# Performance work log

Measured on AMD Instinct MI355X. Metric: run time of the kernel, lower is better.

The kernel has to match this reference:

```python
import jax, jax.numpy as jnp
import numpy as np

B, S, HID = 2, 2048, 2048
H, HKV, D = 16, 4, 128
BS = 64            # block_size
TAU = 0.5          # threshold_tau
NB = S // BS       # number of blocks
SCALE = 1.0 / (D ** 0.5)


def _rotate_half(x):
    x1, x2 = x[..., : D // 2], x[..., D // 2 :]
    return jnp.concatenate([-x2, x1], axis=-1)


def setup_inputs() -> dict:
    key = jax.random.key(0)
    k0, k1, k2, k3, k4 = jax.random.split(key, 5)
    hidden_states = jax.random.normal(k0, (B, S, HID), jnp.float32)
    # standard rotary embeddings, [B, S, D] (ndim==3 path of _apply_rotary_pos_emb)
    pos = jnp.arange(S, dtype=jnp.float32)
    inv_freq = 1.0 / (10000.0 ** (jnp.arange(0, D, 2, dtype=jnp.float32) / D))
    emb = jnp.concatenate([pos[:, None] * inv_freq[None, :]] * 2, axis=-1)  # [S, D]
    cos = jnp.broadcast_to(jnp.cos(emb)[None], (B, S, D)).astype(jnp.float32)
    sin = jnp.broadcast_to(jnp.sin(emb)[None], (B, S, D)).astype(jnp.float32)
    Wq = jax.random.normal(k1, (HID, H * D), jnp.float32) * 0.02
    Wk = jax.random.normal(k2, (HID, HKV * D), jnp.float32) * 0.02
    Wv = jax.random.normal(k3, (HID, HKV * D), jnp.float32) * 0.02
    Wo = jax.random.normal(k4, (HID, HID), jnp.float32) * 0.02
    return {"hidden_states": hidden_states, "cos": cos, "sin": sin,
            "Wq": Wq, "Wk": Wk, "Wv": Wv, "Wo": Wo}


def reference(hidden_states, cos, sin, Wq, Wk, Wv, Wo):
    # QKV projections -> [B, heads, S, D]
    q = (hidden_states @ Wq).reshape(B, S, H, D).transpose(0, 2, 1, 3)
    k = (hidden_states @ Wk).reshape(B, S, HKV, D).transpose(0, 2, 1, 3)
    v = (hidden_states @ Wv).reshape(B, S, HKV, D).transpose(0, 2, 1, 3)
    # RoPE (cos/sin [B,S,D] -> broadcast over heads)
    c, s = cos[:, None], sin[:, None]
    q = q * c + _rotate_half(q) * s
    k = k * c + _rotate_half(k) * s
    # GQA repeat_interleave on head dim
    n_rep = H // HKV
    k = jnp.repeat(k, n_rep, axis=1)
    v = jnp.repeat(v, n_rep, axis=1)
    # ---- AttnGate: block-mean pooled Q/K scores -> hard block mask ----
    q_blk = q.reshape(B, H, NB, BS, D).mean(axis=3)  # [B,H,NB,D]
    k_blk = k.reshape(B, H, NB, BS, D).mean(axis=3)
    gate_logits = jnp.einsum('bhid,bhjd->bhij', q_blk, k_blk) * SCALE
    hard = jax.nn.sigmoid(gate_logits) >= TAU                      # [B,H,NB,NB]
    hard = hard | jnp.eye(NB, dtype=bool)                          # keep diagonal blocks
    hard = hard & jnp.tril(jnp.ones((NB, NB), dtype=bool))         # block-causal
    # expand block mask to token level and intersect with causal mask
    tok_mask = jnp.repeat(jnp.repeat(hard, BS, axis=2), BS, axis=3)  # [B,H,S,S]
    tok_mask = tok_mask & jnp.tril(jnp.ones((S, S), dtype=bool))
    # ---- block-sparse (masked) attention ----
    scores = jnp.einsum('bhsd,bhtd->bhst', q, k) * SCALE
    scores = jnp.where(tok_mask, scores, jnp.float32(-1e30))
    probs = jax.nn.softmax(scores.astype(jnp.float32), axis=-1).astype(v.dtype)
    out = jnp.einsum('bhst,bhtd->bhsd', probs, v)
    out = out.transpose(0, 2, 1, 3).reshape(B, S, HID)
    return out @ Wo
```

## Files before the change

### kernel.cpp

```cpp
#include <hip/hip_runtime.h>
#include <stdint.h>

typedef unsigned short u16;
typedef _Float16 half8 __attribute__((ext_vector_type(8)));
typedef float floatx4 __attribute__((ext_vector_type(4)));
typedef u16 u16x4 __attribute__((ext_vector_type(4)));

#define B_ 2
#define S_ 2048
#define HID_ 2048
#define H_ 16
#define HKV_ 4
#define D_ 128
#define NB_ 32
#define SCALE_ 0.08838834764831845f
#define SC_L2 0.12753102331884178f
#define SMAX_L2 5.770780163555852f

__device__ __forceinline__ u16 f2h_bits(float f) {
  _Float16 h = (_Float16)f;
  return __builtin_bit_cast(u16, h);
}

__global__ __launch_bounds__(256) void k_split_hs(const float* __restrict__ hs, u16* __restrict__ A2) {
  int idx = blockIdx.x * 256 + threadIdx.x;
  int f0 = idx * 4;
  float4 v = *reinterpret_cast<const float4*>(hs + f0);
  float vv[4] = {v.x, v.y, v.z, v.w};
  u16x4 h0, h1;
#pragma unroll
  for (int e = 0; e < 4; ++e) {
    _Float16 a = (_Float16)vv[e];
    float r = vv[e] - (float)a;
    _Float16 b = (_Float16)r;
    h0[e] = __builtin_bit_cast(u16, a);
    h1[e] = __builtin_bit_cast(u16, b);
  }
  int row = f0 >> 11;
  int col = f0 & 2047;
  *reinterpret_cast<u16x4*>(A2 + (size_t)row * 4096 + col) = h0;
  *reinterpret_cast<u16x4*>(A2 + (size_t)row * 4096 + 2048 + col) = h1;
}

__global__ __launch_bounds__(256) void k_transpose_split(const float* __restrict__ src, u16* __restrict__ dst,
                                                         int Kdim, int N, int ldd, int nsplit) {
  __shared__ float tile[64][65];
  int k0 = blockIdx.x * 64, n0 = blockIdx.y * 64;
#pragma unroll
  for (int p = 0; p < 16; ++p) {
    int e = threadIdx.x + p * 256;
    int r = e >> 6, c = e & 63;
    tile[r][c] = src[(size_t)(k0 + r) * N + n0 + c];
  }
  __syncthreads();
#pragma unroll
  for (int p = 0; p < 16; ++p) {
    int e = threadIdx.x + p * 256;
    int k = e & 63, n = e >> 6;
    float v = tile[k][n];
    for (int s = 0; s < nsplit; ++s) {
      _Float16 hh = (_Float16)v;
      dst[(size_t)(n0 + n) * ldd + s * Kdim + k0 + k] = __builtin_bit_cast(u16, hh);
      v -= (float)hh;
    }
  }
}


#define FENCE() __builtin_amdgcn_sched_barrier(0)
#define BAR() do { FENCE(); __builtin_amdgcn_s_barrier(); FENCE(); } while (0)
#define WAITVM(N) do { FENCE(); asm volatile("s_waitcnt vmcnt(" #N ")" ::: "memory"); FENCE(); } while (0)

__device__ __forceinline__ int kmap(int map, int t) {
  return ((map >> ((t >> 5) * 4)) & 15) * 2048 + (t & 31) * 64;
}

__device__ __forceinline__ void stage_half(const u16* __restrict__ src, int sr0, int lda, int kb,
                                           u16* dst, int w, int lane) {
#pragma unroll
  for (int rr = 0; rr < 2; ++rr) {
    int chunk = rr * 8 + w;
    int row = chunk * 8 + (lane >> 3);
    int slot = (lane & 7) ^ (lane >> 3);
    const u16* gp = src + (size_t)(sr0 + row) * lda + kb + slot * 8;
    __builtin_amdgcn_global_load_lds((const __attribute__((address_space(1))) unsigned int*)gp,
                                     (__attribute__((address_space(3))) unsigned int*)(dst + chunk * 512),
                                     16, 0, 0);
  }
}

#define RD_A(mh) do { \
  _Pragma("unroll") \
  for (int m_ = 0; m_ < 4; ++m_) { \
    aF[m_][0] = *reinterpret_cast<const half8*>(&sm[(mh)*8192 + (wm*64 + m_*16 + l15)*64 + ((quad ^ l7) * 8)]); \
    aF[m_][1] = *reinterpret_cast<const half8*>(&sm[(mh)*8192 + (wm*64 + m_*16 + l15)*64 + (((4 + quad) ^ l7) * 8)]); \
  } } while (0)

#define RD_B(nh, BF) do { \
  _Pragma("unroll") \
  for (int n_ = 0; n_ < 2; ++n_) { \
    BF[n_][0] = *reinterpret_cast<const half8*>(&sm[16384 + (nh)*8192 + (wn*32 + n_*16 + l15)*64 + ((quad ^ l7) * 8)]); \
    BF[n_][1] = *reinterpret_cast<const half8*>(&sm[16384 + (nh)*8192 + (wn*32 + n_*16 + l15)*64 + (((4 + quad) ^ l7) * 8)]); \
  } } while (0)

#define MM(mh, nh, BF) do { \
  __builtin_amdgcn_s_setprio(1); \
  _Pragma("unroll") \
  for (int m_ = 0; m_ < 4; ++m_) \
  _Pragma("unroll") \
  for (int n_ = 0; n_ < 2; ++n_) { \
    acc[(mh)*4 + m_][(nh)*2 + n_] = __builtin_amdgcn_mfma_f32_16x16x32_f16(aF[m_][0], BF[n_][0], acc[(mh)*4 + m_][(nh)*2 + n_], 0, 0, 0); \
    acc[(mh)*4 + m_][(nh)*2 + n_] = __builtin_amdgcn_mfma_f32_16x16x32_f16(aF[m_][1], BF[n_][1], acc[(mh)*4 + m_][(nh)*2 + n_], 0, 0, 0); \
  } \
  __builtin_amdgcn_s_setprio(0); } while (0)

__device__ __forceinline__ void gemm256(const u16* __restrict__ A, const u16* __restrict__ BT,
                                        float* __restrict__ C, u16* sm,
                                        int row0, int col0, int NT,
                                        int lda, int ldb, int ldc, int amap, int bmap) {
  const int tid = (int)threadIdx.x;
  const int lane = tid & 63;
  const int w = tid >> 6;
  const int wm = w >> 2, wn = w & 3;
  const int quad = lane >> 4, l15 = lane & 15, l7 = lane & 7;

  floatx4 acc[8][4];
#pragma unroll
  for (int i = 0; i < 8; ++i)
#pragma unroll
    for (int j = 0; j < 4; ++j) acc[i][j] = (floatx4){0.f, 0.f, 0.f, 0.f};

  half8 aF[4][2], bF0[2][2], bF1[2][2];

  {
    int ka = kmap(amap, 0), kb = kmap(bmap, 0);
    stage_half(A,  row0,       lda, ka, sm + 0,     w, lane);
    stage_half(BT, col0,       ldb, kb, sm + 16384, w, lane);
    stage_half(BT, col0 + 128, ldb, kb, sm + 24576, w, lane);
    stage_half(A,  row0 + 128, lda, ka, sm + 8192,  w, lane);
  }
  WAITVM(4);
  BAR();

  for (int t = 0; t < NT; ++t) {
    int tn = t + 1; if (tn >= NT) tn = 0;
    int kan = kmap(amap, tn), kbn = kmap(bmap, tn);

    RD_A(0); RD_B(0, bF0);
    WAITVM(2);
    BAR(); MM(0, 0, bF0); BAR();
    RD_B(1, bF1);
    stage_half(A,  row0, lda, kan, sm + 0,     w, lane);
    stage_half(BT, col0, ldb, kbn, sm + 16384, w, lane);
    WAITVM(4);
    BAR(); MM(0, 1, bF1); BAR();
    RD_A(1);
    stage_half(BT, col0 + 128, ldb, kbn, sm + 24576, w, lane);
    BAR(); MM(1, 1, bF1); BAR();
    stage_half(A, row0 + 128, lda, kan, sm + 8192, w, lane);
    WAITVM(4);
    BAR(); MM(1, 0, bF0); BAR();
  }
  WAITVM(0);

#pragma unroll
  for (int i = 0; i < 8; ++i) {
    int mh = i >> 2, m = i & 3;
#pragma unroll
    for (int j = 0; j < 4; ++j) {
      int nh = j >> 1, n = j & 1;
#pragma unroll
      for (int r = 0; r < 4; ++r) {
        int rr = row0 + mh * 128 + wm * 64 + m * 16 + quad * 4 + r;
        int cc = col0 + nh * 128 + wn * 32 + n * 16 + l15;
        C[(size_t)rr * ldc + cc] = acc[i][j][r];
      }
    }
  }
}

__global__ __launch_bounds__(512) void k_gemm_qkv(const u16* __restrict__ A2, const u16* __restrict__ B2T,
                                                  const u16* __restrict__ WvT, float* __restrict__ qkv) {
  __shared__ u16 sm[32768];
  int id = blockIdx.x;
  int row0, col0, NT, ldb, amap, bmap;
  const u16* Bp;
  float* Cp;
  if (id < 160) {
    row0 = (id / 10) * 256; col0 = (id % 10) * 256;
    NT = 96; ldb = 4096; amap = 0x010; bmap = 0x100;
    Bp = B2T; Cp = qkv;
  } else {
    int t = id - 160;
    row0 = (t >> 1) * 256; col0 = (t & 1) * 256;
    NT = 32; ldb = 2048; amap = 0; bmap = 0;
    Bp = WvT; Cp = qkv + 2560;
  }
  gemm256(A2, Bp, Cp, sm, row0, col0, NT, 4096, ldb, 3072, amap, bmap);
}

__global__ __launch_bounds__(512) void k_gemm_wo(const u16* __restrict__ attn, const u16* __restrict__ WoT,
                                                 float* __restrict__ out) {
  __shared__ u16 sm[32768];
  int id = blockIdx.x;
  gemm256(attn, WoT, out, sm, (id >> 3) * 256, (id & 7) * 256, 32, 2048, 2048, 2048, 0, 0);
}

__global__ __launch_bounds__(256) void k_rope_mean(const float* __restrict__ qkv,
                                                   const float* __restrict__ cosb, const float* __restrict__ sinb,
                                                   u16* __restrict__ qbf, u16* __restrict__ kbf,
                                                   float* __restrict__ qblk, float* __restrict__ kblk) {
  int cc = blockIdx.x, i = blockIdx.y, b = blockIdx.z;
  int c = cc * 256 + threadIdx.x;
  bool isq = c < 2048;
  int hh = isq ? (c >> 7) : ((c - 2048) >> 7);
  int d = isq ? (c & 127) : ((c - 2048) & 127);
  int pairc = (d < 64) ? c + 64 : c - 64;
  float sgn = (d < 64) ? -1.0f : 1.0f;
  int row0 = b * S_ + i * 64;
  float sum = 0.0f;
  for (int s = 0; s < 64; ++s) {
    int row = row0 + s;
    float x1 = qkv[(size_t)row * 3072 + c];
    float x2 = qkv[(size_t)row * 3072 + pairc];
    float cv = cosb[(size_t)row * 128 + d];
    float sv = sinb[(size_t)row * 128 + d];
    float val = x1 * cv + sgn * x2 * sv;
    sum += val;
    if (isq)
      qbf[((size_t)(b * H_ + hh) * S_ + i * 64 + s) * 128 + d] = f2h_bits(val);
    else
      kbf[((size_t)(b * HKV_ + hh) * S_ + i * 64 + s) * 128 + d] = f2h_bits(val);
  }
  if (isq)
    qblk[((size_t)(b * H_ + hh) * NB_ + i) * 128 + d] = sum * 0.015625f;
  else
    kblk[((size_t)(b * HKV_ + hh) * NB_ + i) * 128 + d] = sum * 0.015625f;
}

__global__ __launch_bounds__(256) void k_vlayout(const float* __restrict__ qkv, u16* __restrict__ vT) {
  int i = blockIdx.x, hk = blockIdx.y, b = blockIdx.z;
  __shared__ u16 tile[64 * 130];
#pragma unroll
  for (int p = 0; p < 32; ++p) {
    int e = threadIdx.x + p * 256;
    int s = e >> 7, d = e & 127;
    float v = qkv[(size_t)(b * S_ + i * 64 + s) * 3072 + 2560 + hk * 128 + d];
    tile[s * 130 + d] = f2h_bits(v);
  }
  __syncthreads();
#pragma unroll
  for (int p = 0; p < 32; ++p) {
    int e = threadIdx.x + p * 256;
    int d2 = e >> 6, s2 = e & 63;
    vT[((size_t)(b * HKV_ + hk) * 128 + d2) * S_ + i * 64 + s2] = tile[s2 * 130 + d2];
  }
}

__global__ __launch_bounds__(256) void k_gate(const float* __restrict__ qblk, const float* __restrict__ kblk,
                                              int* __restrict__ mask) {
  int h = blockIdx.x, b = blockIdx.y;
  int hk = h >> 2;
  __shared__ float qs[32 * 128];
  __shared__ float ks[32 * 128];
  size_t qb0 = (size_t)(b * H_ + h) * NB_ * 128;
  size_t kb0 = (size_t)(b * HKV_ + hk) * NB_ * 128;
#pragma unroll
  for (int p = 0; p < 16; ++p) {
    int e = threadIdx.x + p * 256;
    qs[e] = qblk[qb0 + e];
    ks[e] = kblk[kb0 + e];
  }
  __syncthreads();
#pragma unroll
  for (int p = 0; p < 4; ++p) {
    int l = threadIdx.x + p * 256;
    int i = l >> 5, j = l & 31;
    int m;
    if (j > i) m = 0;
    else if (j == i) m = 1;
    else {
      float dot = 0.0f;
      for (int d = 0; d < 128; ++d) dot += qs[i * 128 + d] * ks[j * 128 + d];
      m = (dot >= 0.0f) ? 1 : 0;
    }
    mask[((size_t)(b * H_ + h) * NB_ + i) * NB_ + j] = m;
  }
}

__global__ __launch_bounds__(256) void k_flash(const u16* __restrict__ qbf, const u16* __restrict__ kbf,
                                               const u16* __restrict__ vT, const int* __restrict__ mask,
                                               u16* __restrict__ attn) {
  const int id = blockIdx.x;
  const int i = id >> 5;
  const int hb = id & 31;
  const int h = hb & 15, b = hb >> 4;
  const int hk = h >> 2;
  const int tid = threadIdx.x;
  const int lane = tid & 63;
  const int w = tid >> 6;
  const int quad = lane >> 4;
  const int l15 = lane & 15;

  __shared__ u16 Ks[64 * 128];
  __shared__ u16 Vs[128 * 64];
  __shared__ u16 Ps[4 * 16 * 64];

  half8 qF[4];
  const u16* qbase = qbf + ((size_t)(b * H_ + h) * S_ + i * 64 + w * 16 + l15) * 128;
#pragma unroll
  for (int kk = 0; kk < 4; ++kk)
    qF[kk] = *reinterpret_cast<const half8*>(qbase + kk * 32 + quad * 8);

  floatx4 o[8];
#pragma unroll
  for (int t = 0; t < 8; ++t) o[t] = (floatx4){0.f, 0.f, 0.f, 0.f};
  float ls[4] = {0.f, 0.f, 0.f, 0.f};

  const u16* kb = kbf + (size_t)(b * HKV_ + hk) * S_ * 128;
  const u16* vb = vT + (size_t)(b * HKV_ + hk) * 128 * S_;
  const int* mrp = mask + ((size_t)(b * H_ + h) * NB_ + i) * NB_;

  for (int j = 0; j <= i; ++j) {
    if (!mrp[j]) continue;
#pragma unroll
    for (int t = 0; t < 4; ++t) {
      int g2 = t * 4 + w;
      int stok = g2 * 4 + (lane >> 4);
      int ul = (lane & 15) ^ (stok & 15);
      const u16* srcK = kb + (size_t)(j * 64 + stok) * 128 + ul * 8;
      __builtin_amdgcn_global_load_lds((const __attribute__((address_space(1))) unsigned int*)srcK,
                                       (__attribute__((address_space(3))) unsigned int*)(Ks + g2 * 512),
                                       16, 0, 0);
      int sdd = g2 * 8 + (lane >> 3);
      int ulv = (lane & 7) ^ (sdd & 7);
      const u16* srcV = vb + (size_t)sdd * S_ + j * 64 + ulv * 8;
      __builtin_amdgcn_global_load_lds((const __attribute__((address_space(1))) unsigned int*)srcV,
                                       (__attribute__((address_space(3))) unsigned int*)(Vs + g2 * 512),
                                       16, 0, 0);
    }
    __syncthreads();

#pragma unroll
    for (int ct = 0; ct < 4; ++ct) {
      floatx4 cacc = (floatx4){0.f, 0.f, 0.f, 0.f};
#pragma unroll
      for (int kk = 0; kk < 4; ++kk) {
        int phys = (kk * 4 + quad) ^ l15;
        half8 bF = *reinterpret_cast<const half8*>(&Ks[(ct * 16 + l15) * 128 + phys * 8]);
        cacc = __builtin_amdgcn_mfma_f32_16x16x32_f16(qF[kk], bF, cacc, 0, 0, 0);
      }
#pragma unroll
      for (int r = 0; r < 4; ++r) {
        float s = cacc[r];
        if (j == i && (ct * 16 + l15) > (w * 16 + quad * 4 + r)) s = -1e30f;
        float p = __builtin_exp2f(fmaf(s, SC_L2, -SMAX_L2));
        _Float16 ph = (_Float16)p;
        ls[r] += (float)ph;
        Ps[w * 1024 + (quad * 4 + r) * 64 + ct * 16 + l15] = __builtin_bit_cast(u16, ph);
      }
    }
#pragma unroll
    for (int kk2 = 0; kk2 < 2; ++kk2) {
      half8 aP = *reinterpret_cast<const half8*>(&Ps[w * 1024 + l15 * 64 + kk2 * 32 + quad * 8]);
#pragma unroll
      for (int ct2 = 0; ct2 < 8; ++ct2) {
        int phys = (kk2 * 4 + quad) ^ (l15 & 7);
        half8 bV = *reinterpret_cast<const half8*>(&Vs[(ct2 * 16 + l15) * 64 + phys * 8]);
        o[ct2] = __builtin_amdgcn_mfma_f32_16x16x32_f16(aP, bV, o[ct2], 0, 0, 0);
      }
    }
    __syncthreads();
  }

#pragma unroll
  for (int xm = 1; xm < 16; xm <<= 1)
#pragma unroll
    for (int r = 0; r < 4; ++r) ls[r] += __shfl_xor(ls[r], xm, 64);
  float invl[4];
#pragma unroll
  for (int r = 0; r < 4; ++r) invl[r] = 1.0f / ls[r];
#pragma unroll
  for (int ct2 = 0; ct2 < 8; ++ct2)
#pragma unroll
    for (int r = 0; r < 4; ++r) {
      size_t row = (size_t)(b * S_ + i * 64 + w * 16 + quad * 4 + r);
      attn[row * 2048 + h * 128 + ct2 * 16 + l15] = f2h_bits(o[ct2][r] * invl[r]);
    }
}

extern "C" void kernel_launch(void* const* d_in, const int* in_sizes, int n_in,
                              void* d_out, int out_size, void* d_ws, size_t ws_size,
                              hipStream_t stream) {
  const float* hs = (const float*)d_in[0];
  const float* cosb = (const float*)d_in[1];
  const float* sinb = (const float*)d_in[2];
  const float* Wq = (const float*)d_in[3];
  const float* Wk = (const float*)d_in[4];
  const float* Wv = (const float*)d_in[5];
  const float* Wo = (const float*)d_in[6];
  float* out = (float*)d_out;
  char* ws = (char*)d_ws;

  u16* A2 = (u16*)(ws + 0);
  u16* B2T = (u16*)(ws + 33554432);
  u16* WvT = (u16*)(ws + 54525952);
  float* qkv = (float*)(ws + 56623104);
  u16* attn = (u16*)(ws + 0);
  u16* qbf = (u16*)(ws + 16777216);
  u16* kbf = (u16*)(ws + 33554432);
  u16* vTbf = (u16*)(ws + 37748736);
  float* qblk = (float*)(ws + 41943040);
  float* kblk = (float*)(ws + 42467328);
  int* mask = (int*)(ws + 42598400);
  u16* WoT = (u16*)(ws + 43122688);

  (void)in_sizes; (void)n_in; (void)out_size; (void)ws_size;

  k_split_hs<<<8192, 256, 0, stream>>>(hs, A2);
  k_transpose_split<<<dim3(32, 32), 256, 0, stream>>>(Wq, B2T, 2048, 2048, 4096, 2);
  k_transpose_split<<<dim3(32, 8), 256, 0, stream>>>(Wk, B2T + (size_t)2048 * 4096, 2048, 512, 4096, 2);
  k_transpose_split<<<dim3(32, 8), 256, 0, stream>>>(Wv, WvT, 2048, 512, 2048, 1);

  k_gemm_qkv<<<192, 512, 0, stream>>>(A2, B2T, WvT, qkv);

  k_transpose_split<<<dim3(32, 32), 256, 0, stream>>>(Wo, WoT, 2048, 2048, 2048, 1);

  k_rope_mean<<<dim3(10, 32, 2), 256, 0, stream>>>(qkv, cosb, sinb, qbf, kbf, qblk, kblk);
  k_vlayout<<<dim3(32, 4, 2), 256, 0, stream>>>(qkv, vTbf);

  k_gate<<<dim3(16, 2), 256, 0, stream>>>(qblk, kblk, mask);

  k_flash<<<1024, 256, 0, stream>>>(qbf, kbf, vTbf, mask, attn);

  k_gemm_wo<<<128, 512, 0, stream>>>(attn, WoT, out);
}
```

Measured before the change: 453.0 us.

## Split-K the QKV and Wo GEMMs with atomic accumulation and XCD-aware block remap

The QKV GEMM's three fp16-split K passes become separate workgroups (480 plus 32 for V, launched as 512 blocks), and the Wo GEMM is split into two K halves (256 blocks). Partial results are accumulated with relaxed atomic adds into buffers zeroed by new kernels. Block indices are permuted so that tiles sharing data land on the same XCD. This fills more of the GPU's CUs, at the cost of atomic traffic, two extra zeroing launches, and non-deterministic float summation order.

```diff
diff --git a/kernel.cpp b/kernel.cpp
--- a/kernel.cpp
+++ b/kernel.cpp
@@ -22,6 +22,10 @@
   return __builtin_bit_cast(u16, h);
 }
 
+__global__ __launch_bounds__(256) void k_zero(float4* __restrict__ p) {
+  p[(size_t)blockIdx.x * 256 + threadIdx.x] = (float4){0.f, 0.f, 0.f, 0.f};
+}
+
 __global__ __launch_bounds__(256) void k_split_hs(const float* __restrict__ hs, u16* __restrict__ A2) {
   int idx = blockIdx.x * 256 + threadIdx.x;
   int f0 = idx * 4;
@@ -70,10 +74,6 @@
 #define FENCE() __builtin_amdgcn_sched_barrier(0)
 #define BAR() do { FENCE(); __builtin_amdgcn_s_barrier(); FENCE(); } while (0)
 #define WAITVM(N) do { FENCE(); asm volatile("s_waitcnt vmcnt(" #N ")" ::: "memory"); FENCE(); } while (0)
-
-__device__ __forceinline__ int kmap(int map, int t) {
-  return ((map >> ((t >> 5) * 4)) & 15) * 2048 + (t & 31) * 64;
-}
 
 __device__ __forceinline__ void stage_half(const u16* __restrict__ src, int sr0, int lda, int kb,
                                            u16* dst, int w, int lane) {
@@ -117,7 +117,8 @@
 __device__ __forceinline__ void gemm256(const u16* __restrict__ A, const u16* __restrict__ BT,
                                         float* __restrict__ C, u16* sm,
                                         int row0, int col0, int NT,
-                                        int lda, int ldb, int ldc, int amap, int bmap) {
+                                        int lda, int ldb, int ldc, int koffA, int koffB,
+                                        bool atomicOut) {
   const int tid = (int)threadIdx.x;
   const int lane = tid & 63;
   const int w = tid >> 6;
@@ -133,18 +134,17 @@
   half8 aF[4][2], bF0[2][2], bF1[2][2];
 
   {
-    int ka = kmap(amap, 0), kb = kmap(bmap, 0);
-    stage_half(A,  row0,       lda, ka, sm + 0,     w, lane);
-    stage_half(BT, col0,       ldb, kb, sm + 16384, w, lane);
-    stage_half(BT, col0 + 128, ldb, kb, sm + 24576, w, lane);
-    stage_half(A,  row0 + 128, lda, ka, sm + 8192,  w, lane);
+    stage_half(A,  row0,       lda, koffA, sm + 0,     w, lane);
+    stage_half(BT, col0,       ldb, koffB, sm + 16384, w, lane);
+    stage_half(BT, col0 + 128, ldb, koffB, sm + 24576, w, lane);
+    stage_half(A,  row0 + 128, lda, koffA, sm + 8192,  w, lane);
   }
   WAITVM(4);
   BAR();
 
   for (int t = 0; t < NT; ++t) {
     int tn = t + 1; if (tn >= NT) tn = 0;
-    int kan = kmap(amap, tn), kbn = kmap(bmap, tn);
+    int kan = koffA + tn * 64, kbn = koffB + tn * 64;
 
     RD_A(0); RD_B(0, bF0);
     WAITVM(2);
@@ -173,7 +173,11 @@
       for (int r = 0; r < 4; ++r) {
         int rr = row0 + mh * 128 + wm * 64 + m * 16 + quad * 4 + r;
         int cc = col0 + nh * 128 + wn * 32 + n * 16 + l15;
-        C[(size_t)rr * ldc + cc] = acc[i][j][r];
+        float* cp = C + (size_t)rr * ldc + cc;
+        if (atomicOut)
+          (void)__hip_atomic_fetch_add(cp, acc[i][j][r], __ATOMIC_RELAXED, __HIP_MEMORY_SCOPE_AGENT);
+        else
+          *cp = acc[i][j][r];
       }
     }
   }
@@ -182,28 +186,34 @@
 __global__ __launch_bounds__(512) void k_gemm_qkv(const u16* __restrict__ A2, const u16* __restrict__ B2T,
                                                   const u16* __restrict__ WvT, float* __restrict__ qkv) {
   __shared__ u16 sm[32768];
-  int id = blockIdx.x;
-  int row0, col0, NT, ldb, amap, bmap;
+  int bx = blockIdx.x;
+  int id = ((bx & 7) << 6) | (bx >> 3);
+  int row0, col0, ldb, koffA, koffB;
   const u16* Bp;
   float* Cp;
-  if (id < 160) {
-    row0 = (id / 10) * 256; col0 = (id % 10) * 256;
-    NT = 96; ldb = 4096; amap = 0x010; bmap = 0x100;
-    Bp = B2T; Cp = qkv;
+  bool at;
+  if (id < 480) {
+    int p = id / 160, rem = id % 160;
+    row0 = (rem / 10) * 256; col0 = (rem % 10) * 256;
+    koffA = (p == 1) ? 2048 : 0;
+    koffB = (p == 2) ? 2048 : 0;
+    ldb = 4096; Bp = B2T; Cp = qkv; at = true;
   } else {
-    int t = id - 160;
+    int t = id - 480;
     row0 = (t >> 1) * 256; col0 = (t & 1) * 256;
-    NT = 32; ldb = 2048; amap = 0; bmap = 0;
-    Bp = WvT; Cp = qkv + 2560;
-  }
-  gemm256(A2, Bp, Cp, sm, row0, col0, NT, 4096, ldb, 3072, amap, bmap);
+    koffA = 0; koffB = 0; ldb = 2048; Bp = WvT; Cp = qkv + 2560; at = false;
+  }
+  gemm256(A2, Bp, Cp, sm, row0, col0, 32, 4096, ldb, 3072, koffA, koffB, at);
 }
 
 __global__ __launch_bounds__(512) void k_gemm_wo(const u16* __restrict__ attn, const u16* __restrict__ WoT,
                                                  float* __restrict__ out) {
   __shared__ u16 sm[32768];
-  int id = blockIdx.x;
-  gemm256(attn, WoT, out, sm, (id >> 3) * 256, (id & 7) * 256, 32, 2048, 2048, 2048, 0, 0);
+  int bx = blockIdx.x;
+  int id = ((bx & 7) << 5) | (bx >> 3);
+  int p = id >> 7, rem = id & 127;
+  int row0 = (rem >> 3) * 256, col0 = (rem & 7) * 256;
+  gemm256(attn, WoT, out, sm, row0, col0, 16, 2048, 2048, 2048, p * 1024, p * 1024, true);
 }
 
 __global__ __launch_bounds__(256) void k_rope_mean(const float* __restrict__ qkv,
@@ -417,12 +427,15 @@
 
   (void)in_sizes; (void)n_in; (void)out_size; (void)ws_size;
 
+  k_zero<<<12288, 256, 0, stream>>>((float4*)qkv);
+  k_zero<<<8192, 256, 0, stream>>>((float4*)out);
+
   k_split_hs<<<8192, 256, 0, stream>>>(hs, A2);
   k_transpose_split<<<dim3(32, 32), 256, 0, stream>>>(Wq, B2T, 2048, 2048, 4096, 2);
   k_transpose_split<<<dim3(32, 8), 256, 0, stream>>>(Wk, B2T + (size_t)2048 * 4096, 2048, 512, 4096, 2);
   k_transpose_split<<<dim3(32, 8), 256, 0, stream>>>(Wv, WvT, 2048, 512, 2048, 1);
 
-  k_gemm_qkv<<<192, 512, 0, stream>>>(A2, B2T, WvT, qkv);
+  k_gemm_qkv<<<512, 512, 0, stream>>>(A2, B2T, WvT, qkv);
 
   k_transpose_split<<<dim3(32, 32), 256, 0, stream>>>(Wo, WoT, 2048, 2048, 2048, 1);
 
@@ -433,5 +446,5 @@
 
   k_flash<<<1024, 256, 0, stream>>>(qbf, kbf, vTbf, mask, attn);
 
-  k_gemm_wo<<<128, 512, 0, stream>>>(attn, WoT, out);
-}
+  k_gemm_wo<<<256, 512, 0, stream>>>(attn, WoT, out);
+}
```

New measurement: 520.0 us. +14.8%, slower.

## Split Q/K projection K-loop across extra blocks with fp16 correction buffer

Applied to the files above, without the earlier changes.

The Q/K part of the QKV GEMM, which previously ran a 96-tile split-precision K loop in 160 blocks, is split into two independent workgroup sets. One computes the correction terms (64 tiles) into an fp16 buffer placed in the output allocation, and the other computes the main term (32 tiles) in fp32. The RoPE kernel then adds the correction to the main result. This raises block count from 192 to 352 to fill more CUs and shortens the critical path. In exchange it adds extra fp16 writes and reads, and rounds the correction terms to fp16.

```diff
diff --git a/kernel.cpp b/kernel.cpp
--- a/kernel.cpp
+++ b/kernel.cpp
@@ -115,9 +115,9 @@
   __builtin_amdgcn_s_setprio(0); } while (0)
 
 __device__ __forceinline__ void gemm256(const u16* __restrict__ A, const u16* __restrict__ BT,
-                                        float* __restrict__ C, u16* sm,
+                                        float* __restrict__ C, u16* __restrict__ Ch, u16* sm,
                                         int row0, int col0, int NT,
-                                        int lda, int ldb, int ldc, int amap, int bmap) {
+                                        int lda, int ldb, int ldc, int ldch, int amap, int bmap) {
   const int tid = (int)threadIdx.x;
   const int lane = tid & 63;
   const int w = tid >> 6;
@@ -173,40 +173,43 @@
       for (int r = 0; r < 4; ++r) {
         int rr = row0 + mh * 128 + wm * 64 + m * 16 + quad * 4 + r;
         int cc = col0 + nh * 128 + wn * 32 + n * 16 + l15;
-        C[(size_t)rr * ldc + cc] = acc[i][j][r];
+        if (Ch)
+          Ch[(size_t)rr * ldch + cc] = f2h_bits(acc[i][j][r]);
+        else
+          C[(size_t)rr * ldc + cc] = acc[i][j][r];
       }
     }
   }
 }
 
 __global__ __launch_bounds__(512) void k_gemm_qkv(const u16* __restrict__ A2, const u16* __restrict__ B2T,
-                                                  const u16* __restrict__ WvT, float* __restrict__ qkv) {
+                                                  const u16* __restrict__ WvT, float* __restrict__ qkv,
+                                                  u16* __restrict__ corr) {
   __shared__ u16 sm[32768];
   int id = blockIdx.x;
-  int row0, col0, NT, ldb, amap, bmap;
-  const u16* Bp;
-  float* Cp;
   if (id < 160) {
-    row0 = (id / 10) * 256; col0 = (id % 10) * 256;
-    NT = 96; ldb = 4096; amap = 0x010; bmap = 0x100;
-    Bp = B2T; Cp = qkv;
+    int row0 = (id / 10) * 256, col0 = (id % 10) * 256;
+    gemm256(A2, B2T, nullptr, corr, sm, row0, col0, 64, 4096, 4096, 0, 2560, 0x01, 0x10);
+  } else if (id < 320) {
+    int t = id - 160;
+    int row0 = (t / 10) * 256, col0 = (t % 10) * 256;
+    gemm256(A2, B2T, qkv, nullptr, sm, row0, col0, 32, 4096, 4096, 3072, 0, 0, 0);
   } else {
-    int t = id - 160;
-    row0 = (t >> 1) * 256; col0 = (t & 1) * 256;
-    NT = 32; ldb = 2048; amap = 0; bmap = 0;
-    Bp = WvT; Cp = qkv + 2560;
-  }
-  gemm256(A2, Bp, Cp, sm, row0, col0, NT, 4096, ldb, 3072, amap, bmap);
+    int t = id - 320;
+    int row0 = (t >> 1) * 256, col0 = (t & 1) * 256;
+    gemm256(A2, WvT, qkv + 2560, nullptr, sm, row0, col0, 32, 4096, 2048, 3072, 0, 0, 0);
+  }
 }
 
 __global__ __launch_bounds__(512) void k_gemm_wo(const u16* __restrict__ attn, const u16* __restrict__ WoT,
                                                  float* __restrict__ out) {
   __shared__ u16 sm[32768];
   int id = blockIdx.x;
-  gemm256(attn, WoT, out, sm, (id >> 3) * 256, (id & 7) * 256, 32, 2048, 2048, 2048, 0, 0);
-}
-
-__global__ __launch_bounds__(256) void k_rope_mean(const float* __restrict__ qkv,
+  gemm256(attn, WoT, out, nullptr, sm, (id >> 3) * 256, (id & 7) * 256, 32,
+          2048, 2048, 2048, 0, 0, 0);
+}
+
+__global__ __launch_bounds__(256) void k_rope_mean(const float* __restrict__ qkv, const u16* __restrict__ corr,
                                                    const float* __restrict__ cosb, const float* __restrict__ sinb,
                                                    u16* __restrict__ qbf, u16* __restrict__ kbf,
                                                    float* __restrict__ qblk, float* __restrict__ kblk) {
@@ -221,8 +224,10 @@
   float sum = 0.0f;
   for (int s = 0; s < 64; ++s) {
     int row = row0 + s;
-    float x1 = qkv[(size_t)row * 3072 + c];
-    float x2 = qkv[(size_t)row * 3072 + pairc];
+    float x1 = qkv[(size_t)row * 3072 + c]
+             + (float)__builtin_bit_cast(_Float16, corr[(size_t)row * 2560 + c]);
+    float x2 = qkv[(size_t)row * 3072 + pairc]
+             + (float)__builtin_bit_cast(_Float16, corr[(size_t)row * 2560 + pairc]);
     float cv = cosb[(size_t)row * 128 + d];
     float sv = sinb[(size_t)row * 128 + d];
     float val = x1 * cv + sgn * x2 * sv;
@@ -406,6 +411,7 @@
   u16* B2T = (u16*)(ws + 33554432);
   u16* WvT = (u16*)(ws + 54525952);
   float* qkv = (float*)(ws + 56623104);
+  u16* corr = (u16*)out;
   u16* attn = (u16*)(ws + 0);
   u16* qbf = (u16*)(ws + 16777216);
   u16* kbf = (u16*)(ws + 33554432);
@@ -422,11 +428,11 @@
   k_transpose_split<<<dim3(32, 8), 256, 0, stream>>>(Wk, B2T + (size_t)2048 * 4096, 2048, 512, 4096, 2);
   k_transpose_split<<<dim3(32, 8), 256, 0, stream>>>(Wv, WvT, 2048, 512, 2048, 1);
 
-  k_gemm_qkv<<<192, 512, 0, stream>>>(A2, B2T, WvT, qkv);
+  k_gemm_qkv<<<352, 512, 0, stream>>>(A2, B2T, WvT, qkv, corr);
 
   k_transpose_split<<<dim3(32, 32), 256, 0, stream>>>(Wo, WoT, 2048, 2048, 2048, 1);
 
-  k_rope_mean<<<dim3(10, 32, 2), 256, 0, stream>>>(qkv, cosb, sinb, qbf, kbf, qblk, kblk);
+  k_rope_mean<<<dim3(10, 32, 2), 256, 0, stream>>>(qkv, corr, cosb, sinb, qbf, kbf, qblk, kblk);
   k_vlayout<<<dim3(32, 4, 2), 256, 0, stream>>>(qkv, vTbf);
 
   k_gate<<<dim3(16, 2), 256, 0, stream>>>(qblk, kblk, mask);
```

New measurement: 425.2 us. 1.07x faster.
